# Performance work log

Hardware: AMD Instinct MI355X
Metric: run time of the kernel (lower is better)

Reference implementation:

```python
import jax, jax.numpy as jnp
import numpy as np

B, S, C, H, R, L = 512, 30, 16, 768, 4, 2
EPS = 1e-5


def setup_inputs() -> dict:
    key = jax.random.key(0)
    ks = jax.random.split(key, 12)
    sc = 1.0 / np.sqrt(H)
    return {
        "slots": jax.random.normal(ks[0], (B, S, H), jnp.float32),
        "cls": jax.random.normal(ks[1], (B, C, H), jnp.float32),
        "a_cur": jax.random.uniform(ks[2], (B, S, C), jnp.float32),
        "a_slot": jax.random.uniform(ks[3], (B, S, S), jnp.float32),
        "a_last": jax.random.uniform(ks[4], (B, S, C), jnp.float32),
        "a_dom": jax.random.uniform(ks[5], (B, S, S), jnp.float32),
        "W_r": jax.random.normal(ks[6], (R, H, H), jnp.float32) * sc,
        "b_r": jax.random.normal(ks[7], (R, H), jnp.float32) * sc,
        "W_s": jax.random.normal(ks[8], (H, H), jnp.float32) * sc,
        "b_s": jax.random.normal(ks[9], (H,), jnp.float32) * sc,
        "W_g": jax.random.normal(ks[10], (2 * H, H), jnp.float32) * sc,
        "b_g": jax.random.normal(ks[11], (H,), jnp.float32) * sc,
    }


def reference(slots, cls, a_cur, a_slot, a_last, a_dom, W_r, b_r, W_s, b_s, W_g, b_g):
    for _ in range(L):
        cls_u = cls @ W_s + b_s            # [B,C,H]
        slots_u = slots @ W_s + b_s        # [B,S,H]
        # all R relation projections of both node sets
        rel_cls = jnp.einsum("bch,rhk->rbck", cls, W_r) + b_r[:, None, None, :]
        rel_slots = jnp.einsum("bsh,rhk->rbsk", slots, W_r) + b_r[:, None, None, :]
        # relation 0: updateSlot <-> current turn
        cls_u = cls_u + jnp.einsum("bsc,bsh->bch", a_cur, rel_slots[0]) / (a_cur.sum(-2)[..., None] + EPS)
        slots_u = slots_u + (a_cur @ rel_cls[0]) / (a_cur.sum(-1, keepdims=True) + EPS)
        # relation 1: updateSlot -> all slots
        slots_u = slots_u + (a_slot @ rel_slots[1]) / (a_slot.sum(-1, keepdims=True) + EPS)
        # relation 2: slot <-> last-update turn
        cls_u = cls_u + jnp.einsum("bsc,bsh->bch", a_last, rel_slots[2]) / (a_last.sum(-2)[..., None] + EPS)
        slots_u = slots_u + (a_last @ rel_cls[2]) / (a_last.sum(-1, keepdims=True) + EPS)
        # relation 3: slot-domain connectivity
        slots_u = slots_u + (a_dom @ rel_slots[3]) / (a_dom.sum(-1, keepdims=True) + EPS)
        # gated relu residual update
        gate_slot = jax.nn.sigmoid(jnp.concatenate([slots_u, slots], -1) @ W_g + b_g)
        gate_cls = jax.nn.sigmoid(jnp.concatenate([cls_u, cls], -1) @ W_g + b_g)
        slots = jax.nn.relu(slots_u) * gate_slot + slots * (1.0 - gate_slot)
        cls = jax.nn.relu(cls_u) * gate_cls + cls * (1.0 - gate_cls)
    return cls[:, 1:, :]  # history CLS states [B, C-1, H]
```

## Files before the change

kernel.cpp:

```cpp
#include <hip/hip_runtime.h>
#include <hip/hip_bf16.h>
#include <cstdint>
#include <cstddef>

typedef __hip_bfloat16 bf16;
typedef __bf16 bf16x8 __attribute__((ext_vector_type(8)));
typedef float f32x4 __attribute__((ext_vector_type(4)));

#define S_D 30
#define C_D 16
#define H_D 768
#define EPS_F 1e-5f
#define ISTR 160

__global__ __launch_bounds__(64) void prep_sums_k(
    const float* __restrict__ a_cur, const float* __restrict__ a_slot,
    const float* __restrict__ a_last, const float* __restrict__ a_dom,
    float* __restrict__ ISum)
{
  int b = blockIdx.x, t = threadIdx.x;
  const float* ac  = a_cur  + (size_t)b*S_D*C_D;
  const float* as_ = a_slot + (size_t)b*S_D*S_D;
  const float* al  = a_last + (size_t)b*S_D*C_D;
  const float* ad  = a_dom  + (size_t)b*S_D*S_D;
  float* iv = ISum + (size_t)b*ISTR;
  if (t < S_D) {
    float s1 = 0, s2 = 0, s3 = 0, s4 = 0;
    for (int c = 0; c < C_D; ++c) { s1 += ac[t*C_D+c]; s3 += al[t*C_D+c]; }
    for (int j = 0; j < S_D; ++j) { s2 += as_[t*S_D+j]; s4 += ad[t*S_D+j]; }
    iv[t]      = 1.f/(s1 + EPS_F);
    iv[30 + t] = 1.f/(s3 + EPS_F);
    iv[60 + t] = 1.f/(s2 + EPS_F);
    iv[90 + t] = 1.f/(s4 + EPS_F);
  } else if (t < S_D + C_D) {
    int c = t - S_D;
    float s1 = 0, s3 = 0;
    for (int s = 0; s < S_D; ++s) { s1 += ac[s*C_D+c]; s3 += al[s*C_D+c]; }
    iv[120 + c] = 1.f/(s1 + EPS_F);
    iv[136 + c] = 1.f/(s3 + EPS_F);
  }
}

__global__ __launch_bounds__(256) void prep_weights_k(
    const float* __restrict__ W_r, const float* __restrict__ b_r,
    const float* __restrict__ W_s, const float* __restrict__ b_s,
    const float* __restrict__ W_g,
    bf16* __restrict__ Wcat, bf16* __restrict__ Wg, bf16* __restrict__ Wcat2,
    float* __restrict__ bslot, float* __restrict__ bcls)
{
  int id = blockIdx.x*256 + threadIdx.x;
  const int n1 = 768*3840, n2 = 768*1536, n3 = 768*2304;
  if (id < n1) {
    int n = id / 3840, k = id % 3840, seg = k / 768, kk = k % 768;
    float w = (seg == 0) ? W_s[kk*768 + n] : W_r[((size_t)(seg-1)*768 + kk)*768 + n];
    Wcat[id] = __float2bfloat16(w);
  } else if (id < n1 + n2) {
    int j = id - n1; int n = j / 1536, k = j % 1536;
    Wg[j] = __float2bfloat16(W_g[(size_t)k*768 + n]);
  } else if (id < n1 + n2 + n3) {
    int j = id - n1 - n2; int n = j / 2304, k = j % 2304, seg = k / 768, kk = k % 768;
    float w = (seg == 0) ? W_s[kk*768 + n]
            : (seg == 1 ? W_r[(size_t)kk*768 + n] : W_r[((size_t)2*768 + kk)*768 + n]);
    Wcat2[j] = __float2bfloat16(w);
  } else if (id < n1 + n2 + n3 + 768) {
    int n = id - n1 - n2 - n3;
    bslot[n] = b_s[n] + b_r[n] + b_r[768+n] + b_r[2*768+n] + b_r[3*768+n];
    bcls[n]  = b_s[n] + b_r[n] + b_r[2*768+n];
  }
}

__global__ __launch_bounds__(768) void agg1_k(
    const float* __restrict__ slots, const float* __restrict__ cls,
    const float* __restrict__ a_cur, const float* __restrict__ a_slot,
    const float* __restrict__ a_last, const float* __restrict__ a_dom,
    const float* __restrict__ ISum,
    bf16* __restrict__ Gin, bf16* __restrict__ Zs, bf16* __restrict__ Zc,
    int b0, int rsBase)
{
  int lb = blockIdx.x, b = b0 + lb, h = threadIdx.x;
  float xs[S_D], xc[C_D];
  #pragma unroll
  for (int s = 0; s < S_D; ++s) xs[s] = slots[((size_t)b*S_D + s)*768 + h];
  #pragma unroll
  for (int c = 0; c < C_D; ++c) xc[c] = cls[((size_t)b*C_D + c)*768 + h];

  bf16* Gs = Gin + ((size_t)lb*S_D)*1536 + 768 + h;
  #pragma unroll
  for (int s = 0; s < S_D; ++s) Gs[(size_t)s*1536] = __float2bfloat16(xs[s]);
  bf16* Gc = Gin + ((size_t)(rsBase + lb*C_D))*1536 + 768 + h;
  #pragma unroll
  for (int c = 0; c < C_D; ++c) Gc[(size_t)c*1536] = __float2bfloat16(xc[c]);

  const float* ac  = a_cur  + (size_t)b*S_D*C_D;
  const float* as_ = a_slot + (size_t)b*S_D*S_D;
  const float* al  = a_last + (size_t)b*S_D*C_D;
  const float* ad  = a_dom  + (size_t)b*S_D*S_D;
  const float* iv  = ISum + (size_t)b*ISTR;

  bf16* Zsr = Zs + ((size_t)lb*S_D)*3072 + h;
  #pragma unroll 1
  for (int s = 0; s < S_D; ++s) {
    float a1 = 0, a2 = 0, a3 = 0, a4 = 0;
    #pragma unroll
    for (int c = 0; c < C_D; ++c) { a1 += ac[s*C_D + c]*xc[c]; a3 += al[s*C_D + c]*xc[c]; }
    #pragma unroll
    for (int t = 0; t < S_D; ++t) { a2 += as_[s*S_D + t]*xs[t]; a4 += ad[s*S_D + t]*xs[t]; }
    bf16* row = Zsr + (size_t)s*3072;
    row[0]    = __float2bfloat16(a1*iv[s]);
    row[768]  = __float2bfloat16(a2*iv[60+s]);
    row[1536] = __float2bfloat16(a3*iv[30+s]);
    row[2304] = __float2bfloat16(a4*iv[90+s]);
  }
  bf16* Zcr = Zc + ((size_t)lb*C_D)*1536 + h;
  #pragma unroll 1
  for (int c = 0; c < C_D; ++c) {
    float a1 = 0, a3 = 0;
    #pragma unroll
    for (int s = 0; s < S_D; ++s) { a1 += ac[s*C_D + c]*xs[s]; a3 += al[s*C_D + c]*xs[s]; }
    Zcr[(size_t)c*1536]       = __float2bfloat16(a1*iv[120+c]);
    Zcr[(size_t)c*1536 + 768] = __float2bfloat16(a3*iv[136+c]);
  }
}

__global__ __launch_bounds__(768) void agg2_k(
    const bf16* __restrict__ Xo,
    const float* __restrict__ a_cur, const float* __restrict__ a_last,
    const float* __restrict__ ISum,
    bf16* __restrict__ Gin, bf16* __restrict__ Zc, int b0, int rsBase)
{
  int lb = blockIdx.x, b = b0 + lb, h = threadIdx.x;
  float xs[S_D];
  #pragma unroll
  for (int s = 0; s < S_D; ++s)
    xs[s] = __bfloat162float(Xo[((size_t)(lb*S_D + s))*768 + h]);

  const float* ac = a_cur  + (size_t)b*S_D*C_D;
  const float* al = a_last + (size_t)b*S_D*C_D;
  const float* iv = ISum + (size_t)b*ISTR;

  const bf16* Xc = Xo + ((size_t)(rsBase + lb*C_D))*768 + h;
  bf16* Gc  = Gin + ((size_t)(rsBase + lb*C_D))*1536 + 768 + h;
  bf16* Zcr = Zc + ((size_t)lb*C_D)*1536 + h;
  #pragma unroll 1
  for (int c = 0; c < C_D; ++c) {
    float a1 = 0, a3 = 0;
    #pragma unroll
    for (int s = 0; s < S_D; ++s) { a1 += ac[s*C_D + c]*xs[s]; a3 += al[s*C_D + c]*xs[s]; }
    Zcr[(size_t)c*1536]       = __float2bfloat16(a1*iv[120+c]);
    Zcr[(size_t)c*1536 + 768] = __float2bfloat16(a3*iv[136+c]);
    Gc[(size_t)c*1536] = Xc[(size_t)c*768];
  }
}

template<int K, int EPI, int LDA0, int LDA1, int SK>
__global__ __launch_bounds__(256) void gemm_k(
    const bf16* __restrict__ A0, const bf16* __restrict__ A1,
    const bf16* __restrict__ Bt, bf16* __restrict__ G,
    bf16* __restrict__ Xo, float* __restrict__ out,
    const float* __restrict__ bias, const float* __restrict__ bg, int b0)
{
  __shared__ __align__(16) bf16 As[2][128*64];
  __shared__ __align__(16) bf16 Bs[2][128*64];
  const int tid  = threadIdx.x;
  const int lane = tid & 63;
  const int wave = tid >> 6;
  const int wm = wave >> 1, wn = wave & 1;

  const int nwg = gridDim.x;
  const int q = nwg >> 3, r = nwg & 7;
  const int xcd = blockIdx.x & 7, idx = blockIdx.x >> 3;
  const int wg = (xcd < r ? xcd*(q+1) : r*(q+1) + (xcd-r)*q) + idx;
  const int bm = wg / 6, bn = wg % 6;

  const int swz = (((tid & 7) ^ ((tid >> 3) & 7))) << 3;
  const bf16* Ag0 = A0 + (size_t)(bm*128 + (tid>>3))*LDA0 + swz;
  const bf16* Ag1 = A1 + (size_t)(bm*128 + (tid>>3))*LDA1 + swz;
  const bf16* Bg  = Bt + (size_t)(bn*128 + (tid>>3))*K    + swz;
  const int ldsw = (wave*8)*64;

  f32x4 acc[4][4] = {};
  const int NT = K/64;

  auto stage = [&](int buf, int kt) {
    #pragma unroll
    for (int p = 0; p < 4; ++p) {
      const bf16* asrc = (kt < SK) ? (Ag0 + (size_t)(p*32)*LDA0 + kt)
                                   : (Ag1 + (size_t)(p*32)*LDA1 + (kt - SK));
      __builtin_amdgcn_global_load_lds(
        (const __attribute__((address_space(1))) void*)asrc,
        (__attribute__((address_space(3))) void*)(&As[buf][ldsw + p*32*64]), 16, 0, 0);
      __builtin_amdgcn_global_load_lds(
        (const __attribute__((address_space(1))) void*)(Bg + (size_t)(p*32)*K + kt),
        (__attribute__((address_space(3))) void*)(&Bs[buf][ldsw + p*32*64]), 16, 0, 0);
    }
  };

  stage(0, 0);
  __syncthreads();
  int cur = 0;
  #pragma unroll 1
  for (int t = 0; t < NT; ++t) {
    if (t + 1 < NT) stage(cur ^ 1, (t + 1)*64);
    const bf16* Asb = As[cur];
    const bf16* Bsb = Bs[cur];
    #pragma unroll
    for (int ks = 0; ks < 64; ks += 32) {
      bf16x8 af[4], bfv[4];
      const int sa = ((((ks >> 3) + (lane >> 4)) ^ (lane & 7))) << 3;
      #pragma unroll
      for (int i = 0; i < 4; ++i) {
        int m = wm*64 + i*16 + (lane & 15);
        af[i]  = *(const bf16x8*)&Asb[m*64 + sa];
        int n = wn*64 + i*16 + (lane & 15);
        bfv[i] = *(const bf16x8*)&Bsb[n*64 + sa];
      }
      #pragma unroll
      for (int i = 0; i < 4; ++i)
        #pragma unroll
        for (int j = 0; j < 4; ++j)
          acc[i][j] = __builtin_amdgcn_mfma_f32_16x16x32_bf16(af[i], bfv[j], acc[i][j], 0, 0, 0);
    }
    __syncthreads();
    cur ^= 1;
  }

  const int rbase = bm*128 + wm*64 + ((lane>>4)<<2);
  const int cbase = bn*128 + wn*64 + (lane & 15);
  #pragma unroll
  for (int i = 0; i < 4; ++i) {
    #pragma unroll
    for (int j = 0; j < 4; ++j) {
      const int col = cbase + j*16;
      #pragma unroll
      for (int r2 = 0; r2 < 4; ++r2) {
        const int row = rbase + i*16 + r2;
        float v = acc[i][j][r2];
        if constexpr (EPI == 0) {
          G[(size_t)row*1536 + col] = __float2bfloat16(v + bias[col]);
        } else if constexpr (EPI == 1) {
          v += bg[col];
          float g = 1.f/(1.f + __expf(-v));
          float u = __bfloat162float(G[(size_t)row*1536 + col]);
          float x = __bfloat162float(G[(size_t)row*1536 + 768 + col]);
          Xo[(size_t)row*H_D + col] = __float2bfloat16(fmaxf(u, 0.f)*g + x*(1.f - g));
        } else {
          v += bg[col];
          float g = 1.f/(1.f + __expf(-v));
          float u = __bfloat162float(G[(size_t)row*1536 + col]);
          int bb = row >> 4, c = row & 15;
          if (c >= 1) {
            float x = __bfloat162float(Xo[(size_t)row*H_D + col]);
            out[((size_t)(b0 + bb)*15 + (c - 1))*H_D + col] =
                fmaxf(u, 0.f)*g + x*(1.f - g);
          }
        }
      }
    }
  }
}

extern "C" void kernel_launch(void* const* d_in, const int* in_sizes, int n_in,
                              void* d_out, int out_size, void* d_ws, size_t ws_size,
                              hipStream_t stream)
{
  const float* slots  = (const float*)d_in[0];
  const float* cls    = (const float*)d_in[1];
  const float* a_cur  = (const float*)d_in[2];
  const float* a_slot = (const float*)d_in[3];
  const float* a_last = (const float*)d_in[4];
  const float* a_dom  = (const float*)d_in[5];
  const float* W_r    = (const float*)d_in[6];
  const float* b_r    = (const float*)d_in[7];
  const float* W_s    = (const float*)d_in[8];
  const float* b_s    = (const float*)d_in[9];
  const float* W_g    = (const float*)d_in[10];
  const float* b_g    = (const float*)d_in[11];
  float* out = (float*)d_out;

  char* base = (char*)d_ws;
  size_t off = 0;
  auto alloc = [&](size_t bytes) -> void* {
    void* r = base + off;
    off = (off + bytes + 255) & ~(size_t)255;
    return r;
  };

  float* ISum  = (float*)alloc((size_t)512*ISTR*4);
  bf16* Wcat   = (bf16*)alloc((size_t)768*3840*2);
  bf16* Wg     = (bf16*)alloc((size_t)768*1536*2);
  bf16* Wcat2  = (bf16*)alloc((size_t)768*2304*2);
  float* bslot = (float*)alloc(768*4);
  float* bcls  = (float*)alloc(768*4);
  size_t fixedOff = off;

  const size_t perBatch = (size_t)46*1536*2 + (size_t)46*768*2
                        + (size_t)30*3072*2 + (size_t)16*1536*2;
  int chunkB = 512;
  while (chunkB > 64 && fixedOff + perBatch*(size_t)chunkB + 65536 > ws_size) chunkB >>= 1;

  const int rows_s = chunkB * S_D;
  const int rows_c = chunkB * C_D;
  const int rows_a = chunkB * (S_D + C_D);
  bf16* Gin = (bf16*)alloc((size_t)rows_a*1536*2);
  bf16* Xo  = (bf16*)alloc((size_t)rows_a*768*2);
  bf16* Zs  = (bf16*)alloc((size_t)rows_s*3072*2);
  bf16* Zc  = (bf16*)alloc((size_t)rows_c*1536*2);
  bf16* GinC = Gin + (size_t)rows_s*1536;
  bf16* XoC  = Xo  + (size_t)rows_s*768;

  prep_sums_k<<<512, 64, 0, stream>>>(a_cur, a_slot, a_last, a_dom, ISum);
  {
    int tot = 768*3840 + 768*1536 + 768*2304 + 768;
    prep_weights_k<<<(tot+255)/256, 256, 0, stream>>>(W_r, b_r, W_s, b_s, W_g,
                                                      Wcat, Wg, Wcat2, bslot, bcls);
  }

  for (int b0 = 0; b0 < 512; b0 += chunkB) {
    agg1_k<<<chunkB, 768, 0, stream>>>(slots, cls, a_cur, a_slot, a_last, a_dom,
                                       ISum, Gin, Zs, Zc, b0, rows_s);
    gemm_k<3840, 0, 1536, 3072, 768><<<(rows_s/128)*6, 256, 0, stream>>>(
        Gin + 768, Zs, Wcat, Gin, Xo, out, bslot, b_g, b0);
    gemm_k<2304, 0, 1536, 1536, 768><<<(rows_c/128)*6, 256, 0, stream>>>(
        GinC + 768, Zc, Wcat2, GinC, XoC, out, bcls, b_g, b0);
    gemm_k<1536, 1, 1536, 1536, 1536><<<(rows_a/128)*6, 256, 0, stream>>>(
        Gin, Gin, Wg, Gin, Xo, out, bslot, b_g, b0);
    agg2_k<<<chunkB, 768, 0, stream>>>(Xo, a_cur, a_last, ISum, Gin, Zc, b0, rows_s);
    gemm_k<2304, 0, 1536, 1536, 768><<<(rows_c/128)*6, 256, 0, stream>>>(
        GinC + 768, Zc, Wcat2, GinC, XoC, out, bcls, b_g, b0);
    gemm_k<1536, 2, 1536, 1536, 1536><<<(rows_c/128)*6, 256, 0, stream>>>(
        GinC, GinC, Wg, GinC, XoC, out, bcls, b_g, b0);
  }
}
```

Measured before the change: 615.4 us.

## Pre-normalize adjacency, interleave Z columns, and split aggregation blocks across H

Adjacency matrices are row/column-normalized once in a prep kernel, so the aggregation kernels no longer multiply by inverse sums. The Z operands are laid out interleaved per hidden index (4 relations for slots, 2 for cls), which lets each thread write packed 8-byte or 4-byte stores, and the concatenated weight rows are reordered to match. Aggregation kernels now launch 3x256-thread blocks per batch instead of one 768-thread block, to improve occupancy. The cost is extra workspace for the normalized adjacency copies and a change to the GEMM K ordering that must stay consistent with the weight layout.

```diff
diff --git a/kernel.cpp b/kernel.cpp
--- a/kernel.cpp
+++ b/kernel.cpp
@@ -11,33 +11,39 @@
 #define C_D 16
 #define H_D 768
 #define EPS_F 1e-5f
-#define ISTR 160
-
-__global__ __launch_bounds__(64) void prep_sums_k(
+
+__global__ __launch_bounds__(64) void prep_norm_k(
     const float* __restrict__ a_cur, const float* __restrict__ a_slot,
     const float* __restrict__ a_last, const float* __restrict__ a_dom,
-    float* __restrict__ ISum)
+    float* __restrict__ Acr, float* __restrict__ Acc, float* __restrict__ Asl,
+    float* __restrict__ Alr, float* __restrict__ Alc, float* __restrict__ Adm)
 {
   int b = blockIdx.x, t = threadIdx.x;
   const float* ac  = a_cur  + (size_t)b*S_D*C_D;
   const float* as_ = a_slot + (size_t)b*S_D*S_D;
   const float* al  = a_last + (size_t)b*S_D*C_D;
   const float* ad  = a_dom  + (size_t)b*S_D*S_D;
-  float* iv = ISum + (size_t)b*ISTR;
   if (t < S_D) {
-    float s1 = 0, s2 = 0, s3 = 0, s4 = 0;
-    for (int c = 0; c < C_D; ++c) { s1 += ac[t*C_D+c]; s3 += al[t*C_D+c]; }
-    for (int j = 0; j < S_D; ++j) { s2 += as_[t*S_D+j]; s4 += ad[t*S_D+j]; }
-    iv[t]      = 1.f/(s1 + EPS_F);
-    iv[30 + t] = 1.f/(s3 + EPS_F);
-    iv[60 + t] = 1.f/(s2 + EPS_F);
-    iv[90 + t] = 1.f/(s4 + EPS_F);
+    float s = 0; for (int c=0;c<C_D;c++) s += ac[t*C_D+c];
+    float inv = 1.f/(s+EPS_F);
+    for (int c=0;c<C_D;c++) Acr[(size_t)b*480 + t*C_D+c] = ac[t*C_D+c]*inv;
+    s = 0; for (int c=0;c<C_D;c++) s += al[t*C_D+c];
+    inv = 1.f/(s+EPS_F);
+    for (int c=0;c<C_D;c++) Alr[(size_t)b*480 + t*C_D+c] = al[t*C_D+c]*inv;
+    s = 0; for (int j=0;j<S_D;j++) s += as_[t*S_D+j];
+    inv = 1.f/(s+EPS_F);
+    for (int j=0;j<S_D;j++) Asl[(size_t)b*900 + t*S_D+j] = as_[t*S_D+j]*inv;
+    s = 0; for (int j=0;j<S_D;j++) s += ad[t*S_D+j];
+    inv = 1.f/(s+EPS_F);
+    for (int j=0;j<S_D;j++) Adm[(size_t)b*900 + t*S_D+j] = ad[t*S_D+j]*inv;
   } else if (t < S_D + C_D) {
     int c = t - S_D;
-    float s1 = 0, s3 = 0;
-    for (int s = 0; s < S_D; ++s) { s1 += ac[s*C_D+c]; s3 += al[s*C_D+c]; }
-    iv[120 + c] = 1.f/(s1 + EPS_F);
-    iv[136 + c] = 1.f/(s3 + EPS_F);
+    float s = 0; for (int j=0;j<S_D;j++) s += ac[j*C_D+c];
+    float inv = 1.f/(s+EPS_F);
+    for (int j=0;j<S_D;j++) Acc[(size_t)b*480 + j*C_D+c] = ac[j*C_D+c]*inv;
+    s = 0; for (int j=0;j<S_D;j++) s += al[j*C_D+c];
+    inv = 1.f/(s+EPS_F);
+    for (int j=0;j<S_D;j++) Alc[(size_t)b*480 + j*C_D+c] = al[j*C_D+c]*inv;
   }
 }
 
@@ -51,16 +57,21 @@
   int id = blockIdx.x*256 + threadIdx.x;
   const int n1 = 768*3840, n2 = 768*1536, n3 = 768*2304;
   if (id < n1) {
-    int n = id / 3840, k = id % 3840, seg = k / 768, kk = k % 768;
-    float w = (seg == 0) ? W_s[kk*768 + n] : W_r[((size_t)(seg-1)*768 + kk)*768 + n];
+    int n = id / 3840, k = id % 3840;
+    float w;
+    if (k < 768) w = W_s[k*768 + n];
+    else { int j = k - 768, kk = j >> 2, seg = j & 3;
+           w = W_r[((size_t)seg*768 + kk)*768 + n]; }
     Wcat[id] = __float2bfloat16(w);
   } else if (id < n1 + n2) {
     int j = id - n1; int n = j / 1536, k = j % 1536;
     Wg[j] = __float2bfloat16(W_g[(size_t)k*768 + n]);
   } else if (id < n1 + n2 + n3) {
-    int j = id - n1 - n2; int n = j / 2304, k = j % 2304, seg = k / 768, kk = k % 768;
-    float w = (seg == 0) ? W_s[kk*768 + n]
-            : (seg == 1 ? W_r[(size_t)kk*768 + n] : W_r[((size_t)2*768 + kk)*768 + n]);
+    int j = id - n1 - n2; int n = j / 2304, k = j % 2304;
+    float w;
+    if (k < 768) w = W_s[k*768 + n];
+    else { int jj = k - 768, kk = jj >> 1, seg = jj & 1;
+           w = W_r[((size_t)(seg ? 2 : 0)*768 + kk)*768 + n]; }
     Wcat2[j] = __float2bfloat16(w);
   } else if (id < n1 + n2 + n3 + 768) {
     int n = id - n1 - n2 - n3;
@@ -69,15 +80,16 @@
   }
 }
 
-__global__ __launch_bounds__(768) void agg1_k(
+__global__ __launch_bounds__(256) void agg1_k(
     const float* __restrict__ slots, const float* __restrict__ cls,
-    const float* __restrict__ a_cur, const float* __restrict__ a_slot,
-    const float* __restrict__ a_last, const float* __restrict__ a_dom,
-    const float* __restrict__ ISum,
+    const float* __restrict__ Acr, const float* __restrict__ Acc,
+    const float* __restrict__ Asl, const float* __restrict__ Alr,
+    const float* __restrict__ Alc, const float* __restrict__ Adm,
     bf16* __restrict__ Gin, bf16* __restrict__ Zs, bf16* __restrict__ Zc,
     int b0, int rsBase)
 {
-  int lb = blockIdx.x, b = b0 + lb, h = threadIdx.x;
+  int lb = blockIdx.x, b = b0 + lb;
+  int h = blockIdx.y*256 + threadIdx.x;
   float xs[S_D], xc[C_D];
   #pragma unroll
   for (int s = 0; s < S_D; ++s) xs[s] = slots[((size_t)b*S_D + s)*768 + h];
@@ -91,63 +103,64 @@
   #pragma unroll
   for (int c = 0; c < C_D; ++c) Gc[(size_t)c*1536] = __float2bfloat16(xc[c]);
 
-  const float* ac  = a_cur  + (size_t)b*S_D*C_D;
-  const float* as_ = a_slot + (size_t)b*S_D*S_D;
-  const float* al  = a_last + (size_t)b*S_D*C_D;
-  const float* ad  = a_dom  + (size_t)b*S_D*S_D;
-  const float* iv  = ISum + (size_t)b*ISTR;
-
-  bf16* Zsr = Zs + ((size_t)lb*S_D)*3072 + h;
-  #pragma unroll 1
+  const float* acr = Acr + (size_t)b*480;
+  const float* acc_= Acc + (size_t)b*480;
+  const float* alr = Alr + (size_t)b*480;
+  const float* alc = Alc + (size_t)b*480;
+  const float* asl = Asl + (size_t)b*900;
+  const float* adm = Adm + (size_t)b*900;
+
+  char* Zsr = (char*)(Zs + ((size_t)lb*S_D)*3072 + (size_t)h*4);
   for (int s = 0; s < S_D; ++s) {
     float a1 = 0, a2 = 0, a3 = 0, a4 = 0;
     #pragma unroll
-    for (int c = 0; c < C_D; ++c) { a1 += ac[s*C_D + c]*xc[c]; a3 += al[s*C_D + c]*xc[c]; }
-    #pragma unroll
-    for (int t = 0; t < S_D; ++t) { a2 += as_[s*S_D + t]*xs[t]; a4 += ad[s*S_D + t]*xs[t]; }
-    bf16* row = Zsr + (size_t)s*3072;
-    row[0]    = __float2bfloat16(a1*iv[s]);
-    row[768]  = __float2bfloat16(a2*iv[60+s]);
-    row[1536] = __float2bfloat16(a3*iv[30+s]);
-    row[2304] = __float2bfloat16(a4*iv[90+s]);
-  }
-  bf16* Zcr = Zc + ((size_t)lb*C_D)*1536 + h;
-  #pragma unroll 1
+    for (int c = 0; c < C_D; ++c) { a1 += acr[s*C_D + c]*xc[c]; a3 += alr[s*C_D + c]*xc[c]; }
+    #pragma unroll
+    for (int t = 0; t < S_D; ++t) { a2 += asl[s*S_D + t]*xs[t]; a4 += adm[s*S_D + t]*xs[t]; }
+    union { bf16 hv[4]; uint2 u; } p;
+    p.hv[0] = __float2bfloat16(a1);
+    p.hv[1] = __float2bfloat16(a2);
+    p.hv[2] = __float2bfloat16(a3);
+    p.hv[3] = __float2bfloat16(a4);
+    *(uint2*)(Zsr + (size_t)s*3072*2) = p.u;
+  }
+  char* Zcr = (char*)(Zc + ((size_t)lb*C_D)*1536 + (size_t)h*2);
   for (int c = 0; c < C_D; ++c) {
     float a1 = 0, a3 = 0;
     #pragma unroll
-    for (int s = 0; s < S_D; ++s) { a1 += ac[s*C_D + c]*xs[s]; a3 += al[s*C_D + c]*xs[s]; }
-    Zcr[(size_t)c*1536]       = __float2bfloat16(a1*iv[120+c]);
-    Zcr[(size_t)c*1536 + 768] = __float2bfloat16(a3*iv[136+c]);
-  }
-}
-
-__global__ __launch_bounds__(768) void agg2_k(
+    for (int s = 0; s < S_D; ++s) { a1 += acc_[s*C_D + c]*xs[s]; a3 += alc[s*C_D + c]*xs[s]; }
+    union { bf16 hv[2]; unsigned u; } p;
+    p.hv[0] = __float2bfloat16(a1);
+    p.hv[1] = __float2bfloat16(a3);
+    *(unsigned*)(Zcr + (size_t)c*1536*2) = p.u;
+  }
+}
+
+__global__ __launch_bounds__(256) void agg2_k(
     const bf16* __restrict__ Xo,
-    const float* __restrict__ a_cur, const float* __restrict__ a_last,
-    const float* __restrict__ ISum,
+    const float* __restrict__ Acc, const float* __restrict__ Alc,
     bf16* __restrict__ Gin, bf16* __restrict__ Zc, int b0, int rsBase)
 {
-  int lb = blockIdx.x, b = b0 + lb, h = threadIdx.x;
+  int lb = blockIdx.x, b = b0 + lb;
+  int h = blockIdx.y*256 + threadIdx.x;
   float xs[S_D];
   #pragma unroll
   for (int s = 0; s < S_D; ++s)
     xs[s] = __bfloat162float(Xo[((size_t)(lb*S_D + s))*768 + h]);
 
-  const float* ac = a_cur  + (size_t)b*S_D*C_D;
-  const float* al = a_last + (size_t)b*S_D*C_D;
-  const float* iv = ISum + (size_t)b*ISTR;
-
+  const float* acc_ = Acc + (size_t)b*480;
+  const float* alc  = Alc + (size_t)b*480;
   const bf16* Xc = Xo + ((size_t)(rsBase + lb*C_D))*768 + h;
   bf16* Gc  = Gin + ((size_t)(rsBase + lb*C_D))*1536 + 768 + h;
-  bf16* Zcr = Zc + ((size_t)lb*C_D)*1536 + h;
-  #pragma unroll 1
+  char* Zcr = (char*)(Zc + ((size_t)lb*C_D)*1536 + (size_t)h*2);
   for (int c = 0; c < C_D; ++c) {
     float a1 = 0, a3 = 0;
     #pragma unroll
-    for (int s = 0; s < S_D; ++s) { a1 += ac[s*C_D + c]*xs[s]; a3 += al[s*C_D + c]*xs[s]; }
-    Zcr[(size_t)c*1536]       = __float2bfloat16(a1*iv[120+c]);
-    Zcr[(size_t)c*1536 + 768] = __float2bfloat16(a3*iv[136+c]);
+    for (int s = 0; s < S_D; ++s) { a1 += acc_[s*C_D + c]*xs[s]; a3 += alc[s*C_D + c]*xs[s]; }
+    union { bf16 hv[2]; unsigned u; } p;
+    p.hv[0] = __float2bfloat16(a1);
+    p.hv[1] = __float2bfloat16(a3);
+    *(unsigned*)(Zcr + (size_t)c*1536*2) = p.u;
     Gc[(size_t)c*1536] = Xc[(size_t)c*768];
   }
 }
@@ -285,7 +298,12 @@
     return r;
   };
 
-  float* ISum  = (float*)alloc((size_t)512*ISTR*4);
+  float* Acr = (float*)alloc((size_t)512*480*4);
+  float* Acc = (float*)alloc((size_t)512*480*4);
+  float* Alr = (float*)alloc((size_t)512*480*4);
+  float* Alc = (float*)alloc((size_t)512*480*4);
+  float* Asl = (float*)alloc((size_t)512*900*4);
+  float* Adm = (float*)alloc((size_t)512*900*4);
   bf16* Wcat   = (bf16*)alloc((size_t)768*3840*2);
   bf16* Wg     = (bf16*)alloc((size_t)768*1536*2);
   bf16* Wcat2  = (bf16*)alloc((size_t)768*2304*2);
@@ -308,7 +326,8 @@
   bf16* GinC = Gin + (size_t)rows_s*1536;
   bf16* XoC  = Xo  + (size_t)rows_s*768;
 
-  prep_sums_k<<<512, 64, 0, stream>>>(a_cur, a_slot, a_last, a_dom, ISum);
+  prep_norm_k<<<512, 64, 0, stream>>>(a_cur, a_slot, a_last, a_dom,
+                                      Acr, Acc, Asl, Alr, Alc, Adm);
   {
     int tot = 768*3840 + 768*1536 + 768*2304 + 768;
     prep_weights_k<<<(tot+255)/256, 256, 0, stream>>>(W_r, b_r, W_s, b_s, W_g,
@@ -316,15 +335,15 @@
   }
 
   for (int b0 = 0; b0 < 512; b0 += chunkB) {
-    agg1_k<<<chunkB, 768, 0, stream>>>(slots, cls, a_cur, a_slot, a_last, a_dom,
-                                       ISum, Gin, Zs, Zc, b0, rows_s);
+    agg1_k<<<dim3(chunkB, 3), 256, 0, stream>>>(slots, cls, Acr, Acc, Asl, Alr,
+                                                Alc, Adm, Gin, Zs, Zc, b0, rows_s);
     gemm_k<3840, 0, 1536, 3072, 768><<<(rows_s/128)*6, 256, 0, stream>>>(
         Gin + 768, Zs, Wcat, Gin, Xo, out, bslot, b_g, b0);
     gemm_k<2304, 0, 1536, 1536, 768><<<(rows_c/128)*6, 256, 0, stream>>>(
         GinC + 768, Zc, Wcat2, GinC, XoC, out, bcls, b_g, b0);
     gemm_k<1536, 1, 1536, 1536, 1536><<<(rows_a/128)*6, 256, 0, stream>>>(
         Gin, Gin, Wg, Gin, Xo, out, bslot, b_g, b0);
-    agg2_k<<<chunkB, 768, 0, stream>>>(Xo, a_cur, a_last, ISum, Gin, Zc, b0, rows_s);
+    agg2_k<<<dim3(chunkB, 3), 256, 0, stream>>>(Xo, Acc, Alc, Gin, Zc, b0, rows_s);
     gemm_k<2304, 0, 1536, 1536, 768><<<(rows_c/128)*6, 256, 0, stream>>>(
         GinC + 768, Zc, Wcat2, GinC, XoC, out, bcls, b_g, b0);
     gemm_k<1536, 2, 1536, 1536, 1536><<<(rows_c/128)*6, 256, 0, stream>>>(
```

After: 566.0 us. 8.0% less time.

## Recast per-batch adjacency aggregation as MFMA matmuls with precomputed normalized matrices

Applied to the files above, without the earlier changes.

Replaces the scalar per-thread aggregation kernels with a precomputed bf16 block matrix of row-normalized adjacency coefficients per batch and an MFMA-based kernel that multiplies it against the node features. The normalization sums are folded into that matrix, which removes the separate sums kernel. The gate GEMM epilogue now also writes the updated CLS states into a separate Gin buffer (aliased onto Zs), so the second aggregation kernel no longer has to copy them. The change cuts the scalar FMA work and strided global reads of the old aggregation, at the cost of zero-padded MFMA tiles and a different bf16 rounding order.

```diff
diff --git a/kernel.cpp b/kernel.cpp
--- a/kernel.cpp
+++ b/kernel.cpp
@@ -11,35 +11,6 @@
 #define C_D 16
 #define H_D 768
 #define EPS_F 1e-5f
-#define ISTR 160
-
-__global__ __launch_bounds__(64) void prep_sums_k(
-    const float* __restrict__ a_cur, const float* __restrict__ a_slot,
-    const float* __restrict__ a_last, const float* __restrict__ a_dom,
-    float* __restrict__ ISum)
-{
-  int b = blockIdx.x, t = threadIdx.x;
-  const float* ac  = a_cur  + (size_t)b*S_D*C_D;
-  const float* as_ = a_slot + (size_t)b*S_D*S_D;
-  const float* al  = a_last + (size_t)b*S_D*C_D;
-  const float* ad  = a_dom  + (size_t)b*S_D*S_D;
-  float* iv = ISum + (size_t)b*ISTR;
-  if (t < S_D) {
-    float s1 = 0, s2 = 0, s3 = 0, s4 = 0;
-    for (int c = 0; c < C_D; ++c) { s1 += ac[t*C_D+c]; s3 += al[t*C_D+c]; }
-    for (int j = 0; j < S_D; ++j) { s2 += as_[t*S_D+j]; s4 += ad[t*S_D+j]; }
-    iv[t]      = 1.f/(s1 + EPS_F);
-    iv[30 + t] = 1.f/(s3 + EPS_F);
-    iv[60 + t] = 1.f/(s2 + EPS_F);
-    iv[90 + t] = 1.f/(s4 + EPS_F);
-  } else if (t < S_D + C_D) {
-    int c = t - S_D;
-    float s1 = 0, s3 = 0;
-    for (int s = 0; s < S_D; ++s) { s1 += ac[s*C_D+c]; s3 += al[s*C_D+c]; }
-    iv[120 + c] = 1.f/(s1 + EPS_F);
-    iv[136 + c] = 1.f/(s3 + EPS_F);
-  }
-}
 
 __global__ __launch_bounds__(256) void prep_weights_k(
     const float* __restrict__ W_r, const float* __restrict__ b_r,
@@ -69,86 +40,132 @@
   }
 }
 
-__global__ __launch_bounds__(768) void agg1_k(
-    const float* __restrict__ slots, const float* __restrict__ cls,
+__global__ __launch_bounds__(64) void prep_cmat_k(
     const float* __restrict__ a_cur, const float* __restrict__ a_slot,
     const float* __restrict__ a_last, const float* __restrict__ a_dom,
-    const float* __restrict__ ISum,
-    bf16* __restrict__ Gin, bf16* __restrict__ Zs, bf16* __restrict__ Zc,
-    int b0, int rsBase)
-{
-  int lb = blockIdx.x, b = b0 + lb, h = threadIdx.x;
-  float xs[S_D], xc[C_D];
+    bf16* __restrict__ Cm, bf16* __restrict__ Cm2)
+{
+  __shared__ float ivr[4][S_D];
+  __shared__ float ivc[2][C_D];
+  int b = blockIdx.x, t = threadIdx.x;
+  const float* ac  = a_cur  + (size_t)b*480;
+  const float* as_ = a_slot + (size_t)b*900;
+  const float* al  = a_last + (size_t)b*480;
+  const float* ad  = a_dom  + (size_t)b*900;
+  if (t < S_D) {
+    float s1=0, s2=0, s3=0, s4=0;
+    for (int c=0;c<C_D;c++){ s1+=ac[t*C_D+c]; s3+=al[t*C_D+c]; }
+    for (int j=0;j<S_D;j++){ s2+=as_[t*S_D+j]; s4+=ad[t*S_D+j]; }
+    ivr[0][t]=1.f/(s1+EPS_F); ivr[1][t]=1.f/(s2+EPS_F);
+    ivr[2][t]=1.f/(s3+EPS_F); ivr[3][t]=1.f/(s4+EPS_F);
+  } else if (t < S_D + C_D) {
+    int c = t - S_D; float s1=0, s3=0;
+    for (int j=0;j<S_D;j++){ s1+=ac[j*C_D+c]; s3+=al[j*C_D+c]; }
+    ivc[0][c]=1.f/(s1+EPS_F); ivc[1][c]=1.f/(s3+EPS_F);
+  }
+  __syncthreads();
+  for (int m = t; m < 160; m += 64) {
+    bf16* row = Cm + ((size_t)b*160 + m)*64;
+    uint4 z = {0,0,0,0};
+    #pragma unroll
+    for (int q = 0; q < 8; ++q) *(uint4*)(row + q*8) = z;
+    if (m < 120) {
+      int s = m >> 2, g = m & 3;
+      if (g == 0)      { float iv=ivr[0][s]; for (int c=0;c<C_D;c++) row[30+c]=__float2bfloat16(ac[s*C_D+c]*iv); }
+      else if (g == 1) { float iv=ivr[1][s]; for (int j=0;j<S_D;j++) row[j]   =__float2bfloat16(as_[s*S_D+j]*iv); }
+      else if (g == 2) { float iv=ivr[2][s]; for (int c=0;c<C_D;c++) row[30+c]=__float2bfloat16(al[s*C_D+c]*iv); }
+      else             { float iv=ivr[3][s]; for (int j=0;j<S_D;j++) row[j]   =__float2bfloat16(ad[s*S_D+j]*iv); }
+    } else if (m < 152) {
+      int c = (m-120) >> 1, g = (m-120) & 1;
+      if (g == 0) { float iv=ivc[0][c]; for (int j=0;j<S_D;j++) row[j]=__float2bfloat16(ac[j*C_D+c]*iv); }
+      else        { float iv=ivc[1][c]; for (int j=0;j<S_D;j++) row[j]=__float2bfloat16(al[j*C_D+c]*iv); }
+    }
+  }
+  if (t < 32) {
+    bf16* row = Cm2 + ((size_t)b*32 + t)*32;
+    uint4 z = {0,0,0,0};
+    #pragma unroll
+    for (int q = 0; q < 4; ++q) *(uint4*)(row + q*8) = z;
+    int c = t >> 1, g = t & 1;
+    float iv = g ? ivc[1][c] : ivc[0][c];
+    const float* A = g ? al : ac;
+    for (int j = 0; j < S_D; ++j) row[j] = __float2bfloat16(A[j*C_D+c]*iv);
+  }
+}
+
+template<int MT, int KS, int CVT, int WG>
+__global__ __launch_bounds__(256) void aggmm_k(
+    const bf16* __restrict__ Cm, const float* __restrict__ s0,
+    const float* __restrict__ s1, const bf16* __restrict__ xo,
+    bf16* __restrict__ z0, bf16* __restrict__ z1, bf16* __restrict__ Gin,
+    int b0, int mreal, int z0rows, int rsB)
+{
+  const int bid = blockIdx.x;
+  const int lb = bid >> 1, half = bid & 1, b = b0 + lb;
+  const int tid = threadIdx.x, lane = tid & 63, w = tid >> 6;
+  constexpr int KW = KS*32;
+  const int mr = lane & 15;
+  const int kq = (lane >> 4) << 3;
+
+  bf16x8 af[MT][KS];
+  const bf16* Cb = Cm + (size_t)b*(MT*16)*KW;
   #pragma unroll
-  for (int s = 0; s < S_D; ++s) xs[s] = slots[((size_t)b*S_D + s)*768 + h];
-  #pragma unroll
-  for (int c = 0; c < C_D; ++c) xc[c] = cls[((size_t)b*C_D + c)*768 + h];
-
-  bf16* Gs = Gin + ((size_t)lb*S_D)*1536 + 768 + h;
-  #pragma unroll
-  for (int s = 0; s < S_D; ++s) Gs[(size_t)s*1536] = __float2bfloat16(xs[s]);
-  bf16* Gc = Gin + ((size_t)(rsBase + lb*C_D))*1536 + 768 + h;
-  #pragma unroll
-  for (int c = 0; c < C_D; ++c) Gc[(size_t)c*1536] = __float2bfloat16(xc[c]);
-
-  const float* ac  = a_cur  + (size_t)b*S_D*C_D;
-  const float* as_ = a_slot + (size_t)b*S_D*S_D;
-  const float* al  = a_last + (size_t)b*S_D*C_D;
-  const float* ad  = a_dom  + (size_t)b*S_D*S_D;
-  const float* iv  = ISum + (size_t)b*ISTR;
-
-  bf16* Zsr = Zs + ((size_t)lb*S_D)*3072 + h;
+  for (int m = 0; m < MT; ++m)
+    #pragma unroll
+    for (int ks = 0; ks < KS; ++ks)
+      af[m][ks] = *(const bf16x8*)&Cb[(size_t)(m*16 + mr)*KW + ks*32 + kq];
+
+  const int hb = half*384 + w*96 + mr;
   #pragma unroll 1
-  for (int s = 0; s < S_D; ++s) {
-    float a1 = 0, a2 = 0, a3 = 0, a4 = 0;
-    #pragma unroll
-    for (int c = 0; c < C_D; ++c) { a1 += ac[s*C_D + c]*xc[c]; a3 += al[s*C_D + c]*xc[c]; }
-    #pragma unroll
-    for (int t = 0; t < S_D; ++t) { a2 += as_[s*S_D + t]*xs[t]; a4 += ad[s*S_D + t]*xs[t]; }
-    bf16* row = Zsr + (size_t)s*3072;
-    row[0]    = __float2bfloat16(a1*iv[s]);
-    row[768]  = __float2bfloat16(a2*iv[60+s]);
-    row[1536] = __float2bfloat16(a3*iv[30+s]);
-    row[2304] = __float2bfloat16(a4*iv[90+s]);
-  }
-  bf16* Zcr = Zc + ((size_t)lb*C_D)*1536 + h;
-  #pragma unroll 1
-  for (int c = 0; c < C_D; ++c) {
-    float a1 = 0, a3 = 0;
-    #pragma unroll
-    for (int s = 0; s < S_D; ++s) { a1 += ac[s*C_D + c]*xs[s]; a3 += al[s*C_D + c]*xs[s]; }
-    Zcr[(size_t)c*1536]       = __float2bfloat16(a1*iv[120+c]);
-    Zcr[(size_t)c*1536 + 768] = __float2bfloat16(a3*iv[136+c]);
-  }
-}
-
-__global__ __launch_bounds__(768) void agg2_k(
-    const bf16* __restrict__ Xo,
-    const float* __restrict__ a_cur, const float* __restrict__ a_last,
-    const float* __restrict__ ISum,
-    bf16* __restrict__ Gin, bf16* __restrict__ Zc, int b0, int rsBase)
-{
-  int lb = blockIdx.x, b = b0 + lb, h = threadIdx.x;
-  float xs[S_D];
-  #pragma unroll
-  for (int s = 0; s < S_D; ++s)
-    xs[s] = __bfloat162float(Xo[((size_t)(lb*S_D + s))*768 + h]);
-
-  const float* ac = a_cur  + (size_t)b*S_D*C_D;
-  const float* al = a_last + (size_t)b*S_D*C_D;
-  const float* iv = ISum + (size_t)b*ISTR;
-
-  const bf16* Xc = Xo + ((size_t)(rsBase + lb*C_D))*768 + h;
-  bf16* Gc  = Gin + ((size_t)(rsBase + lb*C_D))*1536 + 768 + h;
-  bf16* Zcr = Zc + ((size_t)lb*C_D)*1536 + h;
-  #pragma unroll 1
-  for (int c = 0; c < C_D; ++c) {
-    float a1 = 0, a3 = 0;
-    #pragma unroll
-    for (int s = 0; s < S_D; ++s) { a1 += ac[s*C_D + c]*xs[s]; a3 += al[s*C_D + c]*xs[s]; }
-    Zcr[(size_t)c*1536]       = __float2bfloat16(a1*iv[120+c]);
-    Zcr[(size_t)c*1536 + 768] = __float2bfloat16(a3*iv[136+c]);
-    Gc[(size_t)c*1536] = Xc[(size_t)c*768];
+  for (int nt = 0; nt < 6; ++nt) {
+    const int h = hb + nt*16;
+    bf16x8 bfr[KS];
+    #pragma unroll
+    for (int ks = 0; ks < KS; ++ks) {
+      union { unsigned short us[8]; bf16x8 v; } tmp;
+      #pragma unroll
+      for (int i = 0; i < 8; ++i) {
+        int k = ks*32 + kq + i;
+        if constexpr (CVT) {
+          bool isl = (k < S_D);
+          int kc = k - S_D; if (kc > C_D-1) kc = C_D-1;
+          float fv = isl ? s0[((size_t)b*S_D + k)*768 + h]
+                         : s1[((size_t)b*C_D + kc)*768 + h];
+          bf16 hv = __float2bfloat16(fv);
+          tmp.us[i] = *(unsigned short*)&hv;
+          if constexpr (WG) {
+            if (k < S_D + C_D) {
+              size_t grow = isl ? ((size_t)lb*S_D + k)
+                                : ((size_t)rsB + (size_t)lb*C_D + (k - S_D));
+              ((unsigned short*)Gin)[grow*1536 + 768 + h] = tmp.us[i];
+            }
+          }
+        } else {
+          int kc = k; if (kc > S_D-1) kc = S_D-1;
+          tmp.us[i] = ((const unsigned short*)xo)[((size_t)lb*S_D + kc)*768 + h];
+        }
+      }
+      bfr[ks] = tmp.v;
+    }
+    #pragma unroll
+    for (int m = 0; m < MT; ++m) {
+      f32x4 acc = {};
+      #pragma unroll
+      for (int ks = 0; ks < KS; ++ks)
+        acc = __builtin_amdgcn_mfma_f32_16x16x32_bf16(af[m][ks], bfr[ks], acc, 0, 0, 0);
+      const int rb = m*16 + ((lane >> 4) << 2);
+      #pragma unroll
+      for (int r = 0; r < 4; ++r) {
+        int mrow = rb + r;
+        if (mrow < mreal) {
+          bf16 ov = __float2bfloat16(acc[r]);
+          bf16* dst = (mrow < z0rows)
+            ? z0 + ((size_t)lb*z0rows + mrow)*768
+            : z1 + ((size_t)lb*32 + (mrow - z0rows))*768;
+          dst[h] = ov;
+        }
+      }
+    }
   }
 }
 
@@ -156,8 +173,9 @@
 __global__ __launch_bounds__(256) void gemm_k(
     const bf16* __restrict__ A0, const bf16* __restrict__ A1,
     const bf16* __restrict__ Bt, bf16* __restrict__ G,
-    bf16* __restrict__ Xo, float* __restrict__ out,
-    const float* __restrict__ bias, const float* __restrict__ bg, int b0)
+    bf16* __restrict__ G2, bf16* __restrict__ Xo, float* __restrict__ out,
+    const float* __restrict__ bias, const float* __restrict__ bg,
+    int b0, int rsB)
 {
   __shared__ __align__(16) bf16 As[2][128*64];
   __shared__ __align__(16) bf16 Bs[2][128*64];
@@ -205,12 +223,12 @@
     const bf16* Bsb = Bs[cur];
     #pragma unroll
     for (int ks = 0; ks < 64; ks += 32) {
-      bf16x8 af[4], bfv[4];
+      bf16x8 afv[4], bfv[4];
       const int sa = ((((ks >> 3) + (lane >> 4)) ^ (lane & 7))) << 3;
       #pragma unroll
       for (int i = 0; i < 4; ++i) {
         int m = wm*64 + i*16 + (lane & 15);
-        af[i]  = *(const bf16x8*)&Asb[m*64 + sa];
+        afv[i] = *(const bf16x8*)&Asb[m*64 + sa];
         int n = wn*64 + i*16 + (lane & 15);
         bfv[i] = *(const bf16x8*)&Bsb[n*64 + sa];
       }
@@ -218,7 +236,7 @@
       for (int i = 0; i < 4; ++i)
         #pragma unroll
         for (int j = 0; j < 4; ++j)
-          acc[i][j] = __builtin_amdgcn_mfma_f32_16x16x32_bf16(af[i], bfv[j], acc[i][j], 0, 0, 0);
+          acc[i][j] = __builtin_amdgcn_mfma_f32_16x16x32_bf16(afv[i], bfv[j], acc[i][j], 0, 0, 0);
     }
     __syncthreads();
     cur ^= 1;
@@ -242,7 +260,10 @@
           float g = 1.f/(1.f + __expf(-v));
           float u = __bfloat162float(G[(size_t)row*1536 + col]);
           float x = __bfloat162float(G[(size_t)row*1536 + 768 + col]);
-          Xo[(size_t)row*H_D + col] = __float2bfloat16(fmaxf(u, 0.f)*g + x*(1.f - g));
+          bf16 nv = __float2bfloat16(fmaxf(u, 0.f)*g + x*(1.f - g));
+          Xo[(size_t)row*H_D + col] = nv;
+          if (row >= rsB)
+            G2[((size_t)(row - rsB))*1536 + 768 + col] = nv;
         } else {
           v += bg[col];
           float g = 1.f/(1.f + __expf(-v));
@@ -285,16 +306,17 @@
     return r;
   };
 
-  float* ISum  = (float*)alloc((size_t)512*ISTR*4);
   bf16* Wcat   = (bf16*)alloc((size_t)768*3840*2);
   bf16* Wg     = (bf16*)alloc((size_t)768*1536*2);
   bf16* Wcat2  = (bf16*)alloc((size_t)768*2304*2);
+  bf16* Cmat   = (bf16*)alloc((size_t)512*160*64*2);
+  bf16* Cmat2  = (bf16*)alloc((size_t)512*32*32*2);
   float* bslot = (float*)alloc(768*4);
   float* bcls  = (float*)alloc(768*4);
   size_t fixedOff = off;
 
   const size_t perBatch = (size_t)46*1536*2 + (size_t)46*768*2
-                        + (size_t)30*3072*2 + (size_t)16*1536*2;
+                        + (size_t)120*768*2 + (size_t)32*768*2;
   int chunkB = 512;
   while (chunkB > 64 && fixedOff + perBatch*(size_t)chunkB + 65536 > ws_size) chunkB >>= 1;
 
@@ -303,31 +325,33 @@
   const int rows_a = chunkB * (S_D + C_D);
   bf16* Gin = (bf16*)alloc((size_t)rows_a*1536*2);
   bf16* Xo  = (bf16*)alloc((size_t)rows_a*768*2);
-  bf16* Zs  = (bf16*)alloc((size_t)rows_s*3072*2);
-  bf16* Zc  = (bf16*)alloc((size_t)rows_c*1536*2);
+  bf16* Zs  = (bf16*)alloc((size_t)chunkB*120*768*2);
+  bf16* Zc  = (bf16*)alloc((size_t)chunkB*32*768*2);
   bf16* GinC = Gin + (size_t)rows_s*1536;
   bf16* XoC  = Xo  + (size_t)rows_s*768;
-
-  prep_sums_k<<<512, 64, 0, stream>>>(a_cur, a_slot, a_last, a_dom, ISum);
+  bf16* GinC2 = Zs;
+
   {
     int tot = 768*3840 + 768*1536 + 768*2304 + 768;
     prep_weights_k<<<(tot+255)/256, 256, 0, stream>>>(W_r, b_r, W_s, b_s, W_g,
                                                       Wcat, Wg, Wcat2, bslot, bcls);
   }
+  prep_cmat_k<<<512, 64, 0, stream>>>(a_cur, a_slot, a_last, a_dom, Cmat, Cmat2);
 
   for (int b0 = 0; b0 < 512; b0 += chunkB) {
-    agg1_k<<<chunkB, 768, 0, stream>>>(slots, cls, a_cur, a_slot, a_last, a_dom,
-                                       ISum, Gin, Zs, Zc, b0, rows_s);
+    aggmm_k<10,2,1,1><<<chunkB*2, 256, 0, stream>>>(
+        Cmat, slots, cls, nullptr, Zs, Zc, Gin, b0, 152, 120, rows_s);
     gemm_k<3840, 0, 1536, 3072, 768><<<(rows_s/128)*6, 256, 0, stream>>>(
-        Gin + 768, Zs, Wcat, Gin, Xo, out, bslot, b_g, b0);
+        Gin + 768, Zs, Wcat, Gin, nullptr, Xo, out, bslot, b_g, b0, 0);
     gemm_k<2304, 0, 1536, 1536, 768><<<(rows_c/128)*6, 256, 0, stream>>>(
-        GinC + 768, Zc, Wcat2, GinC, XoC, out, bcls, b_g, b0);
+        GinC + 768, Zc, Wcat2, GinC, nullptr, XoC, out, bcls, b_g, b0, 0);
     gemm_k<1536, 1, 1536, 1536, 1536><<<(rows_a/128)*6, 256, 0, stream>>>(
-        Gin, Gin, Wg, Gin, Xo, out, bslot, b_g, b0);
-    agg2_k<<<chunkB, 768, 0, stream>>>(Xo, a_cur, a_last, ISum, Gin, Zc, b0, rows_s);
+        Gin, Gin, Wg, Gin, GinC2, Xo, out, bslot, b_g, b0, rows_s);
+    aggmm_k<2,1,0,0><<<chunkB*2, 256, 0, stream>>>(
+        Cmat2, nullptr, nullptr, Xo, Zc, Zc, nullptr, b0, 32, 32, 0);
     gemm_k<2304, 0, 1536, 1536, 768><<<(rows_c/128)*6, 256, 0, stream>>>(
-        GinC + 768, Zc, Wcat2, GinC, XoC, out, bcls, b_g, b0);
+        GinC2 + 768, Zc, Wcat2, GinC2, nullptr, XoC, out, bcls, b_g, b0, 0);
     gemm_k<1536, 2, 1536, 1536, 1536><<<(rows_c/128)*6, 256, 0, stream>>>(
-        GinC, GinC, Wg, GinC, XoC, out, bcls, b_g, b0);
-  }
-}
+        GinC2, GinC2, Wg, GinC2, nullptr, XoC, out, bcls, b_g, b0, 0);
+  }
+}
```

Measured after the change: 670.8 us. 9.0% more time.
